# Kernel optimization log

Measured on AMD Instinct MI355X. Metric: run time of the kernel, lower is better.

The kernel has to match this reference:

```python
import jax, jax.numpy as jnp
import numpy as np

K = 64          # type_num = len(unique(rna_label)); static for jit
TAU = 0.5       # args.info_nce_tau
EPS = 1e-8


def _prototypes(feat, label):
    # per-class mean over the N axis: feat [N,D], label [N] in [0,K)
    s = jax.ops.segment_sum(feat, label, num_segments=K)               # [K,D]
    c = jax.ops.segment_sum(jnp.ones(feat.shape[0], feat.dtype), label, num_segments=K)
    return s / c[:, None]


def _l2norm(x):
    # torch F.normalize(dim=1): x / max(||x||, 1e-12)
    n = jnp.sqrt(jnp.sum(x * x, axis=1, keepdims=True))
    return x / jnp.maximum(n, 1e-12)


def setup_inputs() -> dict:
    key = jax.random.key(0)
    k1, k2, k3, k4 = jax.random.split(key, 4)
    N, D = 100000, 256
    return {
        "atac_feature": jax.random.normal(k1, (N, D), dtype=jnp.float32),
        "rna_feature": jax.random.normal(k2, (N, D), dtype=jnp.float32),
        "atac_label": jax.random.randint(k3, (N,), 0, K, dtype=jnp.int32),
        "rna_label": jax.random.randint(k4, (N,), 0, K, dtype=jnp.int32),
    }


def reference(atac_feature, rna_feature, atac_label, rna_label):
    A = _l2norm(_prototypes(atac_feature, atac_label))   # [K,D]
    R = _l2norm(_prototypes(rna_feature, rna_label))     # [K,D]

    # Fp[k] = exp(A[k] * R[k] / tau), elementwise over D
    Fp = jnp.exp(A * R / TAU)                             # [K,D]

    # pairwise elementwise-product exps: [K,K,D]
    Sa = jnp.exp(A[:, None, :] * A[None, :, :] / TAU)
    Sr = jnp.exp(A[:, None, :] * R[None, :, :] / TAU)

    off = (1.0 - jnp.eye(K, dtype=A.dtype))[:, :, None]   # exclude j == k
    # Fn[k] = sum_{j!=k}(Sa[k,j] + Fp[k]) + sum_{j!=k}(Sr[k,j] + Fp[k])
    Fn = ((Sa + Sr) * off).sum(axis=1) + 2.0 * (K - 1) * Fp

    loss_k = (-jnp.log(Fp / (Fn + EPS))).mean(axis=1)     # [K]
    return loss_k.sum()
```

## Files before the change

kernel.cpp:

```cpp
#include <hip/hip_runtime.h>
#include <math.h>

#define KK 64
#define DD 256
#define GX 256
#define TROWS 32
#define MAXCHUNK 512
#define INV_TAU 2.0f
#define EPSL 1e-8f

typedef __attribute__((address_space(1))) const void gvoid;
typedef __attribute__((address_space(3))) void svoid;


__global__ __launch_bounds__(512, 4) void seg_partial_kernel(
    const float* __restrict__ fa, const float* __restrict__ fr,
    const int* __restrict__ la, const int* __restrict__ lr,
    float* __restrict__ P, float* __restrict__ C, int N)
{
    __shared__ __attribute__((aligned(16))) float stage[2][TROWS * DD];
    __shared__ int lbl[MAXCHUNK];
    __shared__ int cnt[KK];

    const int tid = threadIdx.x;
    const int g = blockIdx.x, f = blockIdx.y;
    const float* __restrict__ feat = f ? fr : fa;
    const int* __restrict__ label = f ? lr : la;

    if (tid < KK) cnt[tid] = 0;

    const int chunk = (N + GX - 1) / GX;
    const int n0 = g * chunk;
    int rows = min(N, n0 + chunk) - n0;
    if (rows < 0) rows = 0;

    __syncthreads();
    for (int i = tid; i < rows; i += 512) lbl[i] = label[n0 + i];
    __syncthreads();
    for (int i = tid; i < rows; i += 512) atomicAdd(&cnt[lbl[i]], 1);

    float accr[8][4];
    #pragma unroll
    for (int i = 0; i < 8; ++i)
        #pragma unroll
        for (int j = 0; j < 4; ++j) accr[i][j] = 0.0f;

    const int nt = (rows + TROWS - 1) / TROWS;
    const int w = tid >> 6, lane = tid & 63;
    const int k0 = 8 * w;
    const size_t limit = (size_t)N * DD - 4;

    #define STAGE(t)                                                                     \
    do {                                                                                 \
        const size_t base_ = ((size_t)(n0 + (t) * TROWS)) * DD + (size_t)w * 1024 + lane * 4; \
        float* lb_ = &stage[(t) & 1][w * 1024];                                          \
        _Pragma("unroll")                                                                \
        for (int i_ = 0; i_ < 4; ++i_) {                                                 \
            size_t e_ = base_ + i_ * 256;                                                \
            if (e_ > limit) e_ = 0;                    \
            __builtin_amdgcn_global_load_lds((gvoid*)(feat + e_), (svoid*)(lb_ + i_ * 256), 16, 0, 0); \
        }                                                                                \
    } while (0)

    if (nt > 0) STAGE(0);
    for (int t = 0; t < nt; ++t) {
        if (t + 1 < nt) {
            STAGE(t + 1);
            asm volatile("s_waitcnt vmcnt(4)" ::: "memory");
        } else {
            asm volatile("s_waitcnt vmcnt(0)" ::: "memory");
        }
        __builtin_amdgcn_s_barrier();

        const int rn = min(TROWS, rows - t * TROWS);
        const float* sb = stage[t & 1];
        const int* lb = lbl + t * TROWS;
        const int myl = (lane < rn) ? lb[lane] : -1;

        #pragma unroll
        for (int i = 0; i < 8; ++i) {
            unsigned long long m = __ballot(myl == (k0 + i));
            while (m) {
                const int r = (int)__builtin_ctzll(m);
                m &= m - 1;
                const float4 v = *(const float4*)(sb + r * DD + 4 * lane);
                accr[i][0] += v.x; accr[i][1] += v.y;
                accr[i][2] += v.z; accr[i][3] += v.w;
            }
        }

        asm volatile("s_waitcnt lgkmcnt(0)" ::: "memory");
        __builtin_amdgcn_s_barrier();
    }

    float* dstb = P + ((size_t)f * GX + g) * (KK * DD);
    #pragma unroll
    for (int i = 0; i < 8; ++i) {
        float4 v = make_float4(accr[i][0], accr[i][1], accr[i][2], accr[i][3]);
        *(float4*)(dstb + (size_t)(k0 + i) * DD + 4 * lane) = v;
    }
    __syncthreads();
    if (tid < KK) C[((size_t)f * GX + g) * KK + tid] = (float)cnt[tid];
    #undef STAGE
}

__global__ __launch_bounds__(256) void proto_norm_kernel(
    const float* __restrict__ P, const float* __restrict__ C,
    float* __restrict__ AR, int G)
{
    const int k = blockIdx.x, f = blockIdx.y, tid = threadIdx.x;
    const float* base = P + (size_t)f * G * (KK * DD) + (size_t)k * DD + tid;

    float s = 0.0f;
    int g = 0;
    for (; g + 8 <= G; g += 8) {
        float v[8];
        #pragma unroll
        for (int u = 0; u < 8; ++u) v[u] = base[(size_t)(g + u) * (KK * DD)];
        #pragma unroll
        for (int u = 0; u < 8; ++u) s += v[u];
    }
    for (; g < G; ++g) s += base[(size_t)g * (KK * DD)];

    float c = 0.0f;
    const float* cb = C + (size_t)f * G * KK + k;
    for (int g2 = 0; g2 < G; ++g2) c += cb[(size_t)g2 * KK];

    const float m = s / c;
    float sq = m * m;
    #pragma unroll
    for (int i = 1; i < 64; i <<= 1) sq += __shfl_xor(sq, i, 64);
    __shared__ float red[4];
    const int wid = tid >> 6, lane = tid & 63;
    if (lane == 0) red[wid] = sq;
    __syncthreads();
    const float nrm = red[0] + red[1] + red[2] + red[3];
    AR[(size_t)f * KK * DD + (size_t)k * DD + tid] = m / fmaxf(sqrtf(nrm), 1e-12f);
}

__global__ __launch_bounds__(256) void loss_kernel(const float* __restrict__ AR,
                                                   float* __restrict__ lossk)
{
    const float* A = AR;
    const float* R = AR + KK * DD;
    const int k = blockIdx.x, tid = threadIdx.x;

    const float a = A[k * DD + tid];
    const float r = R[k * DD + tid];
    const float lfp = a * r * INV_TAU;
    const float fp = expf(lfp);
    float ssa = 0.0f, ssr = 0.0f;
    #pragma unroll 8
    for (int j = 0; j < KK; ++j) {
        ssa += expf(a * A[j * DD + tid] * INV_TAU);
        ssr += expf(a * R[j * DD + tid] * INV_TAU);
    }
    const float Fn = (ssa - expf(a * a * INV_TAU)) + (ssr - fp) + 2.0f * (KK - 1) * fp;
    float l = logf(Fn + EPSL) - lfp;

    #pragma unroll
    for (int i = 1; i < 64; i <<= 1) l += __shfl_xor(l, i, 64);
    __shared__ float red[4];
    const int wid = tid >> 6, lane = tid & 63;
    if (lane == 0) red[wid] = l;
    __syncthreads();
    if (tid == 0) lossk[k] = (red[0] + red[1] + red[2] + red[3]) * (1.0f / DD);
}

__global__ void final_kernel(const float* __restrict__ lossk, float* __restrict__ out)
{
    float v = lossk[threadIdx.x];
    #pragma unroll
    for (int i = 1; i < 64; i <<= 1) v += __shfl_xor(v, i, 64);
    if (threadIdx.x == 0) out[0] = v;
}

extern "C" void kernel_launch(void* const* d_in, const int* in_sizes, int n_in,
                              void* d_out, int out_size, void* d_ws, size_t ws_size,
                              hipStream_t stream)
{
    const float* fa = (const float*)d_in[0];
    const float* fr = (const float*)d_in[1];
    const int* la = (const int*)d_in[2];
    const int* lr = (const int*)d_in[3];
    float* ws = (float*)d_ws;
    float* out = (float*)d_out;
    const int N = in_sizes[2];

    float* P = ws;
    float* C = P + 2L * GX * KK * DD;
    float* AR = C + 2L * GX * KK;
    float* lossk = AR + 2L * KK * DD;

    seg_partial_kernel<<<dim3(GX, 2), 512, 0, stream>>>(fa, fr, la, lr, P, C, N);
    proto_norm_kernel<<<dim3(KK, 2), 256, 0, stream>>>(P, C, AR, GX);
    loss_kernel<<<KK, 256, 0, stream>>>(AR, lossk);
    final_kernel<<<1, 64, 0, stream>>>(lossk, out);
}
```

Baseline: 115.7 us.

## Compute per-class segment sums via bf16 MFMA with one-hot label matrix

Replaces the ballot-driven LDS accumulation in the segment-sum kernel with a matrix multiply: a one-hot label matrix times the feature chunk, run on 32x32x16 bf16 MFMA instructions. Features are loaded directly from global memory into registers with simple double buffering, which removes the LDS staging and its barriers. The aim is to cut the serial per-row accumulation cost. In exchange, features are rounded to bf16 before summation, which lowers precision of the prototypes, and the global loads are column-strided.

```diff
diff --git a/kernel.cpp b/kernel.cpp
--- a/kernel.cpp
+++ b/kernel.cpp
@@ -4,21 +4,27 @@
 #define KK 64
 #define DD 256
 #define GX 256
-#define TROWS 32
+#define CH 16
 #define MAXCHUNK 512
 #define INV_TAU 2.0f
 #define EPSL 1e-8f
 
-typedef __attribute__((address_space(1))) const void gvoid;
-typedef __attribute__((address_space(3))) void svoid;
-
-
-__global__ __launch_bounds__(512, 4) void seg_partial_kernel(
+typedef unsigned int u32;
+typedef __attribute__((ext_vector_type(4))) u32 u32x4;
+typedef __attribute__((ext_vector_type(8))) short s16x8;
+typedef __attribute__((ext_vector_type(16))) float f32x16;
+
+__device__ __forceinline__ u32 f2bf(float f) {
+    u32 u = __builtin_bit_cast(u32, f);
+    return (u + 0x7FFFu + ((u >> 16) & 1u)) >> 16;
+}
+
+
+__global__ __launch_bounds__(512, 4) void seg_mfma_kernel(
     const float* __restrict__ fa, const float* __restrict__ fr,
     const int* __restrict__ la, const int* __restrict__ lr,
     float* __restrict__ P, float* __restrict__ C, int N)
 {
-    __shared__ __attribute__((aligned(16))) float stage[2][TROWS * DD];
     __shared__ int lbl[MAXCHUNK];
     __shared__ int cnt[KK];
 
@@ -29,9 +35,9 @@
 
     if (tid < KK) cnt[tid] = 0;
 
-    const int chunk = (N + GX - 1) / GX;
-    const int n0 = g * chunk;
-    int rows = min(N, n0 + chunk) - n0;
+    const int chunkR = (N + GX - 1) / GX;
+    const int n0 = g * chunkR;
+    int rows = min(N, n0 + chunkR) - n0;
     if (rows < 0) rows = 0;
 
     __syncthreads();
@@ -39,69 +45,77 @@
     __syncthreads();
     for (int i = tid; i < rows; i += 512) atomicAdd(&cnt[lbl[i]], 1);
 
-    float accr[8][4];
-    #pragma unroll
-    for (int i = 0; i < 8; ++i)
-        #pragma unroll
-        for (int j = 0; j < 4; ++j) accr[i][j] = 0.0f;
-
-    const int nt = (rows + TROWS - 1) / TROWS;
     const int w = tid >> 6, lane = tid & 63;
-    const int k0 = 8 * w;
-    const size_t limit = (size_t)N * DD - 4;
-
-    #define STAGE(t)                                                                     \
-    do {                                                                                 \
-        const size_t base_ = ((size_t)(n0 + (t) * TROWS)) * DD + (size_t)w * 1024 + lane * 4; \
-        float* lb_ = &stage[(t) & 1][w * 1024];                                          \
-        _Pragma("unroll")                                                                \
-        for (int i_ = 0; i_ < 4; ++i_) {                                                 \
-            size_t e_ = base_ + i_ * 256;                                                \
-            if (e_ > limit) e_ = 0;                    \
-            __builtin_amdgcn_global_load_lds((gvoid*)(feat + e_), (svoid*)(lb_ + i_ * 256), 16, 0, 0); \
-        }                                                                                \
+    const int half = lane >> 5;
+    const int nn = lane & 31;
+    const int col0 = w * 32;
+
+    f32x16 acc0 = {0.0f}, acc1 = {0.0f};
+
+    const int nfull = rows / CH;
+
+    #define LOADF(dst, t)                                                       \
+    do {                                                                        \
+        const float* bp_ = feat + (size_t)(n0 + (t) * CH + half * 8) * DD + col0 + nn; \
+        _Pragma("unroll")                                                       \
+        for (int j_ = 0; j_ < 8; ++j_) dst[j_] = bp_[j_ * DD];                  \
     } while (0)
 
-    if (nt > 0) STAGE(0);
-    for (int t = 0; t < nt; ++t) {
-        if (t + 1 < nt) {
-            STAGE(t + 1);
-            asm volatile("s_waitcnt vmcnt(4)" ::: "memory");
-        } else {
-            asm volatile("s_waitcnt vmcnt(0)" ::: "memory");
+    #define DO_CHUNK(vc, lv)                                                    \
+    do {                                                                        \
+        u32 a0p[4], a1p[4], bpk[4];                                             \
+        _Pragma("unroll")                                                       \
+        for (int p_ = 0; p_ < 4; ++p_) {                                        \
+            const int j0_ = 2 * p_, j1_ = 2 * p_ + 1;                           \
+            a0p[p_] = ((lv[j0_] == nn)      ? 0x3F80u : 0u) |                   \
+                      ((lv[j1_] == nn)      ? 0x3F800000u : 0u);                \
+            a1p[p_] = ((lv[j0_] == nn + 32) ? 0x3F80u : 0u) |                   \
+                      ((lv[j1_] == nn + 32) ? 0x3F800000u : 0u);                \
+            bpk[p_] = f2bf(vc[j0_]) | (f2bf(vc[j1_]) << 16);                    \
+        }                                                                       \
+        const s16x8 A0 = __builtin_bit_cast(s16x8, (u32x4){a0p[0], a0p[1], a0p[2], a0p[3]}); \
+        const s16x8 A1 = __builtin_bit_cast(s16x8, (u32x4){a1p[0], a1p[1], a1p[2], a1p[3]}); \
+        const s16x8 Bf = __builtin_bit_cast(s16x8, (u32x4){bpk[0], bpk[1], bpk[2], bpk[3]}); \
+        acc0 = __builtin_amdgcn_mfma_f32_32x32x16_bf16(A0, Bf, acc0, 0, 0, 0);  \
+        acc1 = __builtin_amdgcn_mfma_f32_32x32x16_bf16(A1, Bf, acc1, 0, 0, 0);  \
+    } while (0)
+
+    float cur[8], nxt[8];
+    if (nfull > 0) LOADF(cur, 0);
+    for (int t = 0; t < nfull; ++t) {
+        if (t + 1 < nfull) LOADF(nxt, t + 1);
+        int lv[8];
+        const int r0 = t * CH + half * 8;
+        #pragma unroll
+        for (int j = 0; j < 8; ++j) lv[j] = lbl[r0 + j];
+        DO_CHUNK(cur, lv);
+        #pragma unroll
+        for (int j = 0; j < 8; ++j) cur[j] = nxt[j];
+    }
+    if (nfull * CH < rows) {
+        const int r0 = nfull * CH + half * 8;
+        float tv[8];
+        int lv[8];
+        #pragma unroll
+        for (int j = 0; j < 8; ++j) {
+            const int rr = r0 + j;
+            lv[j] = (rr < rows) ? lbl[rr] : -1;
+            tv[j] = feat[(size_t)(n0 + ((rr < rows) ? rr : 0)) * DD + col0 + nn];
         }
-        __builtin_amdgcn_s_barrier();
-
-        const int rn = min(TROWS, rows - t * TROWS);
-        const float* sb = stage[t & 1];
-        const int* lb = lbl + t * TROWS;
-        const int myl = (lane < rn) ? lb[lane] : -1;
-
-        #pragma unroll
-        for (int i = 0; i < 8; ++i) {
-            unsigned long long m = __ballot(myl == (k0 + i));
-            while (m) {
-                const int r = (int)__builtin_ctzll(m);
-                m &= m - 1;
-                const float4 v = *(const float4*)(sb + r * DD + 4 * lane);
-                accr[i][0] += v.x; accr[i][1] += v.y;
-                accr[i][2] += v.z; accr[i][3] += v.w;
-            }
-        }
-
-        asm volatile("s_waitcnt lgkmcnt(0)" ::: "memory");
-        __builtin_amdgcn_s_barrier();
-    }
+        DO_CHUNK(tv, lv);
+    }
+    #undef LOADF
+    #undef DO_CHUNK
 
     float* dstb = P + ((size_t)f * GX + g) * (KK * DD);
     #pragma unroll
-    for (int i = 0; i < 8; ++i) {
-        float4 v = make_float4(accr[i][0], accr[i][1], accr[i][2], accr[i][3]);
-        *(float4*)(dstb + (size_t)(k0 + i) * DD + 4 * lane) = v;
+    for (int rg = 0; rg < 16; ++rg) {
+        const int cls = (rg & 3) + 8 * (rg >> 2) + 4 * half;
+        dstb[(size_t)cls * DD + col0 + nn] = acc0[rg];
+        dstb[(size_t)(cls + 32) * DD + col0 + nn] = acc1[rg];
     }
     __syncthreads();
     if (tid < KK) C[((size_t)f * GX + g) * KK + tid] = (float)cnt[tid];
-    #undef STAGE
 }
 
 __global__ __launch_bounds__(256) void proto_norm_kernel(
@@ -192,7 +206,7 @@
     float* AR = C + 2L * GX * KK;
     float* lossk = AR + 2L * KK * DD;
 
-    seg_partial_kernel<<<dim3(GX, 2), 512, 0, stream>>>(fa, fr, la, lr, P, C, N);
+    seg_mfma_kernel<<<dim3(GX, 2), 512, 0, stream>>>(fa, fr, la, lr, P, C, N);
     proto_norm_kernel<<<dim3(KK, 2), 256, 0, stream>>>(P, C, AR, GX);
     loss_kernel<<<KK, 256, 0, stream>>>(AR, lossk);
     final_kernel<<<1, 64, 0, stream>>>(lossk, out);
```

New measurement: 117.4 us. Within noise of the previous version (+1.5%).
